# Performance work log

Measured on AMD Instinct MI355X. Metric: run time of the kernel, lower is better.

The kernel has to match this reference:

```python
import jax, jax.numpy as jnp
import numpy as np


def setup_inputs() -> dict:
    key = jax.random.key(0)
    ks = jax.random.split(key, 5)
    B, N, Fin, Fout = 8, 2048, 512, 512
    stdv = 1.0 / np.sqrt(Fout)
    w_stdv = 1.0 / np.sqrt(Fin)
    x = jax.random.normal(ks[0], (B, N, Fin), dtype=jnp.float32)
    weight = jax.random.uniform(ks[1], (Fin, Fout), dtype=jnp.float32, minval=-stdv, maxval=stdv)
    bias = jax.random.uniform(ks[2], (Fout,), dtype=jnp.float32, minval=-stdv, maxval=stdv)
    w_one = jax.random.uniform(ks[3], (Fin, Fin), dtype=jnp.float32, minval=-w_stdv, maxval=w_stdv)
    w_two = jax.random.uniform(ks[4], (Fin, Fin), dtype=jnp.float32, minval=-w_stdv, maxval=w_stdv)
    return {"x": x, "weight": weight, "bias": bias, "w_one": w_one, "w_two": w_two}


def reference(x, weight, bias, w_one, w_two):
    # x: [B, N, Fin]
    support = jnp.einsum('bnf,fo->bno', x, weight)          # [B, N, Fout]
    phi_one = jnp.einsum('ef,bnf->ben', w_one, x)           # [B, Fin, N]
    phi_two = jnp.einsum('ef,bnf->ben', w_two, x)           # [B, Fin, N]
    adj = jnp.einsum('ben,bem->bnm', phi_one, phi_two)      # [B, N, N]
    adj = jax.nn.softmax(adj, axis=1)                        # softmax over dim=1 (columns)
    out = jnp.einsum('bnm,bmo->bno', adj, support)           # [B, N, Fout]
    return out + bias
```

## Files before the change

kernel.cpp:

```cpp
#include <hip/hip_runtime.h>
#include <math.h>

#define BB 8
#define NN 2048
#define FF 512
#define LOG2E 1.4426950408889634f

typedef __attribute__((ext_vector_type(8))) short short8;
typedef __attribute__((ext_vector_type(4))) float floatx4;
typedef __attribute__((ext_vector_type(2))) float float2v;
typedef __attribute__((ext_vector_type(2))) __bf16 bf16x2;

__device__ __forceinline__ unsigned short f2bf(float f) {
    union { float f; unsigned u; } v; v.f = f;
    unsigned r = v.u + 0x7FFFu + ((v.u >> 16) & 1u);
    return (unsigned short)(r >> 16);
}

__device__ __forceinline__ float fexp2(float x) {
#if __has_builtin(__builtin_amdgcn_exp2f)
    return __builtin_amdgcn_exp2f(x);
#else
    return __expf(x * 0.69314718056f);
#endif
}

__device__ __forceinline__ void pk_store(unsigned short* p0, unsigned short* p1,
                                         float a, float b) {
    union { bf16x2 h; unsigned short s[2]; } u;
    float2v v; v.x = a; v.y = b;
    u.h = __builtin_convertvector(v, bf16x2);
    *p0 = u.s[0]; *p1 = u.s[1];
}

__global__ __launch_bounds__(256) void gemm_mfma_bt(
    const unsigned short* __restrict__ A, const unsigned short* __restrict__ B,
    void* __restrict__ Cv, const float* __restrict__ bias, float* __restrict__ Dsum,
    int M, int Nc, int K, int a_ld, int b_ld, int ldc,
    long a_batch, long b_batch, long c_batch, int mode)
{
    __shared__ __align__(16) unsigned short Alds[128 * 64];
    __shared__ __align__(16) unsigned short Blds[128 * 64];

    const int tid  = threadIdx.x;
    const int wave = tid >> 6;
    const int lane = tid & 63;
    const int bz   = blockIdx.z;

    const int m0 = blockIdx.y * 128;
    const int n0 = blockIdx.x * 128;

    const unsigned short* Aptr = A + (long)bz * a_batch + (long)m0 * a_ld;
    const unsigned short* Bptr = B + (long)bz * b_batch + (long)n0 * b_ld;

    const int wm   = (wave >> 1) * 64;
    const int wn   = (wave & 1) * 64;
    const int fl   = lane & 15;
    const int quad = lane >> 4;

    int offA[4], offB[4], cb[4];
    #pragma unroll
    for (int issue = 0; issue < 4; ++issue) {
        const int cbase = issue * 256 + wave * 64;
        const int c = cbase + lane;
        const int row = c >> 3;
        const int kq = ((c & 7) ^ ((c >> 3) & 7)) * 8;
        offA[issue] = row * a_ld + kq;
        offB[issue] = row * b_ld + kq;
        cb[issue] = cbase * 8;
    }

    floatx4 acc[4][4] = {};

    for (int k0 = 0; k0 < K; k0 += 64) {
        #pragma unroll
        for (int issue = 0; issue < 4; ++issue) {
            __builtin_amdgcn_global_load_lds(
                (const __attribute__((address_space(1))) void*)(Aptr + offA[issue]),
                (__attribute__((address_space(3))) void*)&Alds[cb[issue]], 16, 0, 0);
            __builtin_amdgcn_global_load_lds(
                (const __attribute__((address_space(1))) void*)(Bptr + offB[issue]),
                (__attribute__((address_space(3))) void*)&Blds[cb[issue]], 16, 0, 0);
        }
        Aptr += 64; Bptr += 64;
        __syncthreads();

        #pragma unroll
        for (int s = 0; s < 2; ++s) {
            short8 af[4], bf[4];
            const int slot = ((s * 4 + quad) ^ (fl & 7)) * 8;
            #pragma unroll
            for (int i = 0; i < 4; ++i)
                af[i] = *(const short8*)&Alds[(wm + i * 16 + fl) * 64 + slot];
            #pragma unroll
            for (int j = 0; j < 4; ++j)
                bf[j] = *(const short8*)&Blds[(wn + j * 16 + fl) * 64 + slot];
            #pragma unroll
            for (int i = 0; i < 4; ++i)
                #pragma unroll
                for (int j = 0; j < 4; ++j)
                    acc[i][j] = __builtin_amdgcn_mfma_f32_16x16x32_bf16(af[i], bf[j], acc[i][j], 0, 0, 0);
        }
        __syncthreads();
    }

    if (mode == 0) {
        float* Cb = (float*)Cv + (long)bz * c_batch;
        #pragma unroll
        for (int j = 0; j < 4; ++j) {
            const int ng = n0 + wn + j * 16 + fl;
            const float badd = bias ? bias[ng] : 0.0f;
            #pragma unroll
            for (int i = 0; i < 4; ++i) {
                const int mg = m0 + wm + i * 16 + quad * 4;
                #pragma unroll
                for (int r = 0; r < 4; ++r)
                    Cb[(long)(mg + r) * ldc + ng] = acc[i][j][r] + badd;
            }
        }
    } else if (mode == 1) {
        unsigned short* Cb = (unsigned short*)Cv + (long)bz * c_batch;
        #pragma unroll
        for (int j = 0; j < 4; ++j) {
            const int ng = n0 + wn + j * 16 + fl;
            #pragma unroll
            for (int i = 0; i < 4; ++i) {
                const int mg = m0 + wm + i * 16 + quad * 4;
                pk_store(&Cb[(long)(mg + 0) * ldc + ng], &Cb[(long)(mg + 1) * ldc + ng],
                         acc[i][j][0], acc[i][j][1]);
                pk_store(&Cb[(long)(mg + 2) * ldc + ng], &Cb[(long)(mg + 3) * ldc + ng],
                         acc[i][j][2], acc[i][j][3]);
            }
        }
    } else {
        unsigned short* Cb = (unsigned short*)Cv + (long)bz * c_batch;
        float* Db = Dsum + (long)bz * NN;
        #pragma unroll
        for (int i = 0; i < 4; ++i)
            #pragma unroll
            for (int j = 0; j < 4; ++j)
                #pragma unroll
                for (int r = 0; r < 4; ++r)
                    acc[i][j][r] = fexp2(acc[i][j][r]);
        #pragma unroll
        for (int j = 0; j < 4; ++j) {
            const int ng = n0 + wn + j * 16 + fl;
            float csum = 0.f;
            #pragma unroll
            for (int i = 0; i < 4; ++i) {
                const int mg = m0 + wm + i * 16 + quad * 4;
                csum += acc[i][j][0] + acc[i][j][1] + acc[i][j][2] + acc[i][j][3];
                pk_store(&Cb[(long)(mg + 0) * ldc + ng], &Cb[(long)(mg + 1) * ldc + ng],
                         acc[i][j][0], acc[i][j][1]);
                pk_store(&Cb[(long)(mg + 2) * ldc + ng], &Cb[(long)(mg + 3) * ldc + ng],
                         acc[i][j][2], acc[i][j][3]);
            }
            csum += __shfl_xor(csum, 16);
            csum += __shfl_xor(csum, 32);
            if (quad == 0) atomicAdd(&Db[ng], csum);
        }
    }
}

__global__ __launch_bounds__(256) void convert_all(
    const float* __restrict__ x, const float* __restrict__ w1, const float* __restrict__ w2,
    unsigned short* __restrict__ xb, unsigned short* __restrict__ w1b, unsigned short* __restrict__ w2b)
{
    const long NX = (long)BB * NN * FF / 8;
    const long NW = (long)FF * FF / 8;
    long t = (long)blockIdx.x * 256 + threadIdx.x;
    const float* in; unsigned short* out; float sc = 1.0f;
    if (t < NX) { in = x; out = xb; }
    else if (t < NX + NW) { in = w1; out = w1b; t -= NX; sc = LOG2E; }
    else if (t < NX + 2 * NW) { in = w2; out = w2b; t -= NX + NW; }
    else return;
    const long i = t * 8;
    float4 a = *(const float4*)(in + i);
    float4 b = *(const float4*)(in + i + 4);
    union { bf16x2 h[4]; short8 s8; } u;
    float2v v;
    v.x = a.x * sc; v.y = a.y * sc; u.h[0] = __builtin_convertvector(v, bf16x2);
    v.x = a.z * sc; v.y = a.w * sc; u.h[1] = __builtin_convertvector(v, bf16x2);
    v.x = b.x * sc; v.y = b.y * sc; u.h[2] = __builtin_convertvector(v, bf16x2);
    v.x = b.z * sc; v.y = b.w * sc; u.h[3] = __builtin_convertvector(v, bf16x2);
    *(short8*)(out + i) = u.s8;
}

__global__ __launch_bounds__(256) void transpose_convert(
    const float* __restrict__ in, unsigned short* __restrict__ out, int dim)
{
    __shared__ float t[32][33];
    const int tx = threadIdx.x & 31, ty = threadIdx.x >> 5;
    const int x0 = blockIdx.x * 32, y0 = blockIdx.y * 32;
    #pragma unroll
    for (int k = 0; k < 32; k += 8)
        t[ty + k][tx] = in[(long)(y0 + ty + k) * dim + x0 + tx];
    __syncthreads();
    #pragma unroll
    for (int k = 0; k < 32; k += 8)
        out[(long)(x0 + ty + k) * dim + y0 + tx] = f2bf(t[tx][ty + k]);
}

__global__ __launch_bounds__(256) void zero_f32(float* __restrict__ p, long n)
{
    long i = (long)blockIdx.x * 256 + threadIdx.x;
    if (i < n) p[i] = 0.0f;
}

__global__ __launch_bounds__(256) void scale_transpose(
    const unsigned short* __restrict__ Call, const float* __restrict__ D,
    unsigned short* __restrict__ supT, int batch0)
{
    __shared__ float t[32][33];
    __shared__ float rD[32];
    const int tx = threadIdx.x & 31, ty = threadIdx.x >> 5;
    const int mt = blockIdx.x * 32, ot = blockIdx.y * 32;
    const int b = batch0 + blockIdx.z;
    const unsigned short* Cb = Call + (long)b * NN * 1536;
    unsigned short* Tb = supT + (long)b * NN * FF;
    if (threadIdx.x < 32) rD[threadIdx.x] = 1.0f / D[(long)b * NN + mt + threadIdx.x];
    __syncthreads();
    #pragma unroll
    for (int k = 0; k < 32; k += 8) {
        unsigned short u = Cb[(long)(mt + ty + k) * 1536 + 1024 + ot + tx];
        union { unsigned uu; float f; } cv; cv.uu = ((unsigned)u) << 16;
        t[ty + k][tx] = cv.f;
    }
    __syncthreads();
    #pragma unroll
    for (int k = 0; k < 32; k += 8)
        Tb[(long)(ot + ty + k) * NN + mt + tx] = f2bf(t[tx][ty + k] * rD[tx]);
}

extern "C" void kernel_launch(void* const* d_in, const int* in_sizes, int n_in,
                              void* d_out, int out_size, void* d_ws, size_t ws_size,
                              hipStream_t stream)
{
    const float* x      = (const float*)d_in[0];
    const float* weight = (const float*)d_in[1];
    const float* bias   = (const float*)d_in[2];
    const float* w_one  = (const float*)d_in[3];
    const float* w_two  = (const float*)d_in[4];
    float* out = (float*)d_out;

    const long NF  = (long)NN * FF;
    const long NN2 = (long)NN * NN;
    const long CROW = 1536;

    char* p = (char*)d_ws;
    unsigned short* xb    = (unsigned short*)p; p += (size_t)BB * NF * 2;
    unsigned short* Wall  = (unsigned short*)p; p += (size_t)CROW * FF * 2;
    unsigned short* Call  = (unsigned short*)p; p += (size_t)BB * NN * CROW * 2;
    unsigned short* supT  = (unsigned short*)p; p += (size_t)BB * NF * 2;
    float*          Dsum  = (float*)p;          p += (size_t)BB * NN * 4;
    unsigned short* E     = (unsigned short*)p;
    unsigned short* w1b = Wall;
    unsigned short* w2b = Wall + (size_t)FF * FF;
    unsigned short* wTb = Wall + (size_t)2 * FF * FF;

    const size_t fixed = (size_t)(p - (char*)d_ws);
    const bool full = ws_size >= fixed + (size_t)BB * NN2 * 2;

    dim3 blk(256);

    convert_all<<<dim3(4352), blk, 0, stream>>>(x, w_one, w_two, xb, w1b, w2b);
    transpose_convert<<<dim3(FF / 32, FF / 32), blk, 0, stream>>>(weight, wTb, FF);
    zero_f32<<<dim3((BB * NN) / 256), blk, 0, stream>>>(Dsum, BB * NN);

    gemm_mfma_bt<<<dim3(CROW / 128, NN / 128, BB), blk, 0, stream>>>(
        xb, Wall, Call, nullptr, nullptr, NN, (int)CROW, FF,
        FF, FF, (int)CROW, NF, 0, NN * CROW, 1);

    if (full) {
        gemm_mfma_bt<<<dim3(NN / 128, NN / 128, BB), blk, 0, stream>>>(
            Call, Call + FF, E, nullptr, Dsum, NN, NN, FF,
            (int)CROW, (int)CROW, NN, NN * CROW, NN * CROW, NN2, 2);
        scale_transpose<<<dim3(NN / 32, FF / 32, BB), blk, 0, stream>>>(Call, Dsum, supT, 0);
        gemm_mfma_bt<<<dim3(FF / 128, NN / 128, BB), blk, 0, stream>>>(
            E, supT, out, bias, nullptr, NN, FF, NN,
            NN, NN, FF, NN2, NF, NF, 0);
    } else {
        for (int b = 0; b < BB; ++b) {
            const unsigned short* Cb = Call + (size_t)b * NN * CROW;
            gemm_mfma_bt<<<dim3(NN / 128, NN / 128, 1), blk, 0, stream>>>(
                Cb, Cb + FF, E, nullptr, Dsum + (size_t)b * NN, NN, NN, FF,
                (int)CROW, (int)CROW, NN, 0, 0, 0, 2);
            scale_transpose<<<dim3(NN / 32, FF / 32, 1), blk, 0, stream>>>(Call, Dsum, supT, b);
            gemm_mfma_bt<<<dim3(FF / 128, NN / 128, 1), blk, 0, stream>>>(
                E, supT + (size_t)b * NF, out + (size_t)b * NF, bias, nullptr, NN, FF, NN,
                NN, NN, FF, 0, 0, 0, 0);
        }
    }
}
```

Measured before the change: 240.6 us.

## Switch GEMMs to 32x32x16 MFMA with templated block tiles

Replaces the 16x16x32 bf16 MFMA kernel with a templated kernel that uses 32x32x16 MFMA instructions, each wave computing a 64x64 tile as 2x2 fragments. The template makes the block shape configurable: the first two GEMMs now use 8 waves with 256x128 tiles, and the final GEMM keeps 128x128 with 4 waves. Larger MFMA fragments mean fewer LDS fragment loads per FLOP, and the bigger tiles give more data reuse. The cost is more LDS per block and different occupancy. Epilogue indexing is rewritten to match the 32x32 accumulator layout.

```diff
diff --git a/kernel.cpp b/kernel.cpp
--- a/kernel.cpp
+++ b/kernel.cpp
@@ -7,7 +7,7 @@
 #define LOG2E 1.4426950408889634f
 
 typedef __attribute__((ext_vector_type(8))) short short8;
-typedef __attribute__((ext_vector_type(4))) float floatx4;
+typedef __attribute__((ext_vector_type(16))) float floatx16;
 typedef __attribute__((ext_vector_type(2))) float float2v;
 typedef __attribute__((ext_vector_type(2))) __bf16 bf16x2;
 
@@ -33,73 +33,85 @@
     *p0 = u.s[0]; *p1 = u.s[1];
 }
 
-__global__ __launch_bounds__(256) void gemm_mfma_bt(
+template<int WI, int WJ>
+__global__ __launch_bounds__(WI * WJ * 64) void gemm32(
     const unsigned short* __restrict__ A, const unsigned short* __restrict__ B,
     void* __restrict__ Cv, const float* __restrict__ bias, float* __restrict__ Dsum,
-    int M, int Nc, int K, int a_ld, int b_ld, int ldc,
+    int K, int a_ld, int b_ld, int ldc,
     long a_batch, long b_batch, long c_batch, int mode)
 {
-    __shared__ __align__(16) unsigned short Alds[128 * 64];
-    __shared__ __align__(16) unsigned short Blds[128 * 64];
+    constexpr int TI = WI * 64, TJ = WJ * 64, NT = WI * WJ * 64;
+    constexpr int AISS = TI * 8 / NT;
+    constexpr int BISS = TJ * 8 / NT;
+
+    __shared__ __align__(16) unsigned short Alds[TI * 64];
+    __shared__ __align__(16) unsigned short Blds[TJ * 64];
 
     const int tid  = threadIdx.x;
     const int wave = tid >> 6;
     const int lane = tid & 63;
     const int bz   = blockIdx.z;
 
-    const int m0 = blockIdx.y * 128;
-    const int n0 = blockIdx.x * 128;
+    const int m0 = blockIdx.y * TI;
+    const int n0 = blockIdx.x * TJ;
 
     const unsigned short* Aptr = A + (long)bz * a_batch + (long)m0 * a_ld;
     const unsigned short* Bptr = B + (long)bz * b_batch + (long)n0 * b_ld;
 
-    const int wm   = (wave >> 1) * 64;
-    const int wn   = (wave & 1) * 64;
-    const int fl   = lane & 15;
-    const int quad = lane >> 4;
-
-    int offA[4], offB[4], cb[4];
-    #pragma unroll
-    for (int issue = 0; issue < 4; ++issue) {
-        const int cbase = issue * 256 + wave * 64;
+    const int wi = wave / WJ, wj = wave % WJ;
+    const int wm = wi * 64, wn = wj * 64;
+    const int l31 = lane & 31;
+    const int lh  = lane >> 5;
+
+    int offA[AISS], cbA[AISS], offB[BISS], cbB[BISS];
+    #pragma unroll
+    for (int s = 0; s < AISS; ++s) {
+        const int cbase = s * NT + wave * 64;
         const int c = cbase + lane;
-        const int row = c >> 3;
-        const int kq = ((c & 7) ^ ((c >> 3) & 7)) * 8;
-        offA[issue] = row * a_ld + kq;
-        offB[issue] = row * b_ld + kq;
-        cb[issue] = cbase * 8;
-    }
-
-    floatx4 acc[4][4] = {};
+        offA[s] = (c >> 3) * a_ld + (((c & 7) ^ ((c >> 3) & 7)) << 3);
+        cbA[s] = cbase * 8;
+    }
+    #pragma unroll
+    for (int s = 0; s < BISS; ++s) {
+        const int cbase = s * NT + wave * 64;
+        const int c = cbase + lane;
+        offB[s] = (c >> 3) * b_ld + (((c & 7) ^ ((c >> 3) & 7)) << 3);
+        cbB[s] = cbase * 8;
+    }
+
+    floatx16 acc[2][2] = {};
 
     for (int k0 = 0; k0 < K; k0 += 64) {
         #pragma unroll
-        for (int issue = 0; issue < 4; ++issue) {
+        for (int s = 0; s < AISS; ++s)
             __builtin_amdgcn_global_load_lds(
-                (const __attribute__((address_space(1))) void*)(Aptr + offA[issue]),
-                (__attribute__((address_space(3))) void*)&Alds[cb[issue]], 16, 0, 0);
+                (const __attribute__((address_space(1))) void*)(Aptr + offA[s]),
+                (__attribute__((address_space(3))) void*)&Alds[cbA[s]], 16, 0, 0);
+        #pragma unroll
+        for (int s = 0; s < BISS; ++s)
             __builtin_amdgcn_global_load_lds(
-                (const __attribute__((address_space(1))) void*)(Bptr + offB[issue]),
-                (__attribute__((address_space(3))) void*)&Blds[cb[issue]], 16, 0, 0);
-        }
+                (const __attribute__((address_space(1))) void*)(Bptr + offB[s]),
+                (__attribute__((address_space(3))) void*)&Blds[cbB[s]], 16, 0, 0);
         Aptr += 64; Bptr += 64;
         __syncthreads();
 
         #pragma unroll
-        for (int s = 0; s < 2; ++s) {
-            short8 af[4], bf[4];
-            const int slot = ((s * 4 + quad) ^ (fl & 7)) * 8;
-            #pragma unroll
-            for (int i = 0; i < 4; ++i)
-                af[i] = *(const short8*)&Alds[(wm + i * 16 + fl) * 64 + slot];
-            #pragma unroll
-            for (int j = 0; j < 4; ++j)
-                bf[j] = *(const short8*)&Blds[(wn + j * 16 + fl) * 64 + slot];
-            #pragma unroll
-            for (int i = 0; i < 4; ++i)
-                #pragma unroll
-                for (int j = 0; j < 4; ++j)
-                    acc[i][j] = __builtin_amdgcn_mfma_f32_16x16x32_bf16(af[i], bf[j], acc[i][j], 0, 0, 0);
+        for (int ks = 0; ks < 4; ++ks) {
+            const int kc = ks * 2 + lh;
+            const int sw = (kc ^ (lane & 7)) << 3;
+            short8 af[2], bf[2];
+            #pragma unroll
+            for (int fi = 0; fi < 2; ++fi)
+                af[fi] = *(const short8*)&Alds[(wm + fi * 32 + l31) * 64 + sw];
+            #pragma unroll
+            for (int fj = 0; fj < 2; ++fj)
+                bf[fj] = *(const short8*)&Blds[(wn + fj * 32 + l31) * 64 + sw];
+            #pragma unroll
+            for (int fi = 0; fi < 2; ++fi)
+                #pragma unroll
+                for (int fj = 0; fj < 2; ++fj)
+                    acc[fi][fj] = __builtin_amdgcn_mfma_f32_32x32x16_bf16(
+                        af[fi], bf[fj], acc[fi][fj], 0, 0, 0);
         }
         __syncthreads();
     }
@@ -107,57 +119,64 @@
     if (mode == 0) {
         float* Cb = (float*)Cv + (long)bz * c_batch;
         #pragma unroll
-        for (int j = 0; j < 4; ++j) {
-            const int ng = n0 + wn + j * 16 + fl;
-            const float badd = bias ? bias[ng] : 0.0f;
-            #pragma unroll
-            for (int i = 0; i < 4; ++i) {
-                const int mg = m0 + wm + i * 16 + quad * 4;
-                #pragma unroll
-                for (int r = 0; r < 4; ++r)
-                    Cb[(long)(mg + r) * ldc + ng] = acc[i][j][r] + badd;
+        for (int fj = 0; fj < 2; ++fj) {
+            const int j = n0 + wn + fj * 32 + l31;
+            const float badd = bias ? bias[j] : 0.0f;
+            #pragma unroll
+            for (int fi = 0; fi < 2; ++fi) {
+                const int ib = m0 + wm + fi * 32 + 4 * lh;
+                #pragma unroll
+                for (int r = 0; r < 16; ++r) {
+                    const int i = ib + (r & 3) + 8 * (r >> 2);
+                    Cb[(long)i * ldc + j] = acc[fi][fj][r] + badd;
+                }
             }
         }
     } else if (mode == 1) {
         unsigned short* Cb = (unsigned short*)Cv + (long)bz * c_batch;
         #pragma unroll
-        for (int j = 0; j < 4; ++j) {
-            const int ng = n0 + wn + j * 16 + fl;
-            #pragma unroll
-            for (int i = 0; i < 4; ++i) {
-                const int mg = m0 + wm + i * 16 + quad * 4;
-                pk_store(&Cb[(long)(mg + 0) * ldc + ng], &Cb[(long)(mg + 1) * ldc + ng],
-                         acc[i][j][0], acc[i][j][1]);
-                pk_store(&Cb[(long)(mg + 2) * ldc + ng], &Cb[(long)(mg + 3) * ldc + ng],
-                         acc[i][j][2], acc[i][j][3]);
+        for (int fj = 0; fj < 2; ++fj) {
+            const int j = n0 + wn + fj * 32 + l31;
+            #pragma unroll
+            for (int fi = 0; fi < 2; ++fi) {
+                const int ib = m0 + wm + fi * 32 + 4 * lh;
+                #pragma unroll
+                for (int r = 0; r < 16; r += 2) {
+                    const int i0 = ib + ((r) & 3) + 8 * ((r) >> 2);
+                    const int i1 = ib + ((r + 1) & 3) + 8 * ((r + 1) >> 2);
+                    pk_store(&Cb[(long)i0 * ldc + j], &Cb[(long)i1 * ldc + j],
+                             acc[fi][fj][r], acc[fi][fj][r + 1]);
+                }
             }
         }
     } else {
         unsigned short* Cb = (unsigned short*)Cv + (long)bz * c_batch;
         float* Db = Dsum + (long)bz * NN;
         #pragma unroll
-        for (int i = 0; i < 4; ++i)
-            #pragma unroll
-            for (int j = 0; j < 4; ++j)
-                #pragma unroll
-                for (int r = 0; r < 4; ++r)
-                    acc[i][j][r] = fexp2(acc[i][j][r]);
-        #pragma unroll
-        for (int j = 0; j < 4; ++j) {
-            const int ng = n0 + wn + j * 16 + fl;
+        for (int fi = 0; fi < 2; ++fi)
+            #pragma unroll
+            for (int fj = 0; fj < 2; ++fj)
+                #pragma unroll
+                for (int r = 0; r < 16; ++r)
+                    acc[fi][fj][r] = fexp2(acc[fi][fj][r]);
+        #pragma unroll
+        for (int fj = 0; fj < 2; ++fj) {
+            const int j = n0 + wn + fj * 32 + l31;
             float csum = 0.f;
             #pragma unroll
-            for (int i = 0; i < 4; ++i) {
-                const int mg = m0 + wm + i * 16 + quad * 4;
-                csum += acc[i][j][0] + acc[i][j][1] + acc[i][j][2] + acc[i][j][3];
-                pk_store(&Cb[(long)(mg + 0) * ldc + ng], &Cb[(long)(mg + 1) * ldc + ng],
-                         acc[i][j][0], acc[i][j][1]);
-                pk_store(&Cb[(long)(mg + 2) * ldc + ng], &Cb[(long)(mg + 3) * ldc + ng],
-                         acc[i][j][2], acc[i][j][3]);
+            for (int fi = 0; fi < 2; ++fi) {
+                const int ib = m0 + wm + fi * 32 + 4 * lh;
+                #pragma unroll
+                for (int r = 0; r < 16; r += 2) {
+                    const int i0 = ib + ((r) & 3) + 8 * ((r) >> 2);
+                    const int i1 = ib + ((r + 1) & 3) + 8 * ((r + 1) >> 2);
+                    pk_store(&Cb[(long)i0 * ldc + j], &Cb[(long)i1 * ldc + j],
+                             acc[fi][fj][r], acc[fi][fj][r + 1]);
+                    csum += acc[fi][fj][r] + acc[fi][fj][r + 1];
+                }
             }
-            csum += __shfl_xor(csum, 16);
             csum += __shfl_xor(csum, 32);
-            if (quad == 0) atomicAdd(&Db[ng], csum);
+            if (lh == 0) atomicAdd(&Db[j], csum);
         }
     }
 }
@@ -267,27 +286,27 @@
     transpose_convert<<<dim3(FF / 32, FF / 32), blk, 0, stream>>>(weight, wTb, FF);
     zero_f32<<<dim3((BB * NN) / 256), blk, 0, stream>>>(Dsum, BB * NN);
 
-    gemm_mfma_bt<<<dim3(CROW / 128, NN / 128, BB), blk, 0, stream>>>(
-        xb, Wall, Call, nullptr, nullptr, NN, (int)CROW, FF,
+    gemm32<4, 2><<<dim3(CROW / 128, NN / 256, BB), dim3(512), 0, stream>>>(
+        xb, Wall, Call, nullptr, nullptr, FF,
         FF, FF, (int)CROW, NF, 0, NN * CROW, 1);
 
     if (full) {
-        gemm_mfma_bt<<<dim3(NN / 128, NN / 128, BB), blk, 0, stream>>>(
-            Call, Call + FF, E, nullptr, Dsum, NN, NN, FF,
+        gemm32<4, 2><<<dim3(NN / 128, NN / 256, BB), dim3(512), 0, stream>>>(
+            Call, Call + FF, E, nullptr, Dsum, FF,
             (int)CROW, (int)CROW, NN, NN * CROW, NN * CROW, NN2, 2);
         scale_transpose<<<dim3(NN / 32, FF / 32, BB), blk, 0, stream>>>(Call, Dsum, supT, 0);
-        gemm_mfma_bt<<<dim3(FF / 128, NN / 128, BB), blk, 0, stream>>>(
-            E, supT, out, bias, nullptr, NN, FF, NN,
+        gemm32<2, 2><<<dim3(FF / 128, NN / 128, BB), blk, 0, stream>>>(
+            E, supT, out, bias, nullptr, NN,
             NN, NN, FF, NN2, NF, NF, 0);
     } else {
         for (int b = 0; b < BB; ++b) {
             const unsigned short* Cb = Call + (size_t)b * NN * CROW;
-            gemm_mfma_bt<<<dim3(NN / 128, NN / 128, 1), blk, 0, stream>>>(
-                Cb, Cb + FF, E, nullptr, Dsum + (size_t)b * NN, NN, NN, FF,
+            gemm32<4, 2><<<dim3(NN / 128, NN / 256, 1), dim3(512), 0, stream>>>(
+                Cb, Cb + FF, E, nullptr, Dsum + (size_t)b * NN, FF,
                 (int)CROW, (int)CROW, NN, 0, 0, 0, 2);
             scale_transpose<<<dim3(NN / 32, FF / 32, 1), blk, 0, stream>>>(Call, Dsum, supT, b);
-            gemm_mfma_bt<<<dim3(FF / 128, NN / 128, 1), blk, 0, stream>>>(
-                E, supT + (size_t)b * NF, out + (size_t)b * NF, bias, nullptr, NN, FF, NN,
+            gemm32<2, 2><<<dim3(FF / 128, NN / 128, 1), blk, 0, stream>>>(
+                E, supT + (size_t)b * NF, out + (size_t)b * NF, bias, nullptr, NN,
                 NN, NN, FF, 0, 0, 0, 0);
         }
     }
```

Result: slower. 250.2 us (+4.0%).

## Use two-wave 128x128 GEMM blocks with 128x64 per-wave tiles

Applied to the files above, without the earlier changes.

The GEMM kernel now runs with 128 threads (2 waves) per 128x128 tile instead of 4 waves. Each wave computes a 128x64 sub-tile with an 8x4 grid of 16x16 MFMA accumulators. This raises the MFMA-to-LDS-read ratio, since A fragments are shared across more B fragments, and launch bounds request 2 blocks per CU. The trade-off is doubled accumulator register pressure and fewer waves per block for hiding latency, with each thread issuing twice as many global-to-LDS loads.

```diff
diff --git a/kernel.cpp b/kernel.cpp
--- a/kernel.cpp
+++ b/kernel.cpp
@@ -33,10 +33,10 @@
     *p0 = u.s[0]; *p1 = u.s[1];
 }
 
-__global__ __launch_bounds__(256) void gemm_mfma_bt(
+__global__ __launch_bounds__(128, 2) void gemm_bt16(
     const unsigned short* __restrict__ A, const unsigned short* __restrict__ B,
     void* __restrict__ Cv, const float* __restrict__ bias, float* __restrict__ Dsum,
-    int M, int Nc, int K, int a_ld, int b_ld, int ldc,
+    int K, int a_ld, int b_ld, int ldc,
     long a_batch, long b_batch, long c_batch, int mode)
 {
     __shared__ __align__(16) unsigned short Alds[128 * 64];
@@ -53,50 +53,47 @@
     const unsigned short* Aptr = A + (long)bz * a_batch + (long)m0 * a_ld;
     const unsigned short* Bptr = B + (long)bz * b_batch + (long)n0 * b_ld;
 
-    const int wm   = (wave >> 1) * 64;
-    const int wn   = (wave & 1) * 64;
+    const int wn   = wave * 64;
     const int fl   = lane & 15;
     const int quad = lane >> 4;
 
-    int offA[4], offB[4], cb[4];
-    #pragma unroll
-    for (int issue = 0; issue < 4; ++issue) {
-        const int cbase = issue * 256 + wave * 64;
-        const int c = cbase + lane;
+    int offA[8], offB[8];
+    #pragma unroll
+    for (int s = 0; s < 8; ++s) {
+        const int c = s * 128 + tid;
         const int row = c >> 3;
-        const int kq = ((c & 7) ^ ((c >> 3) & 7)) * 8;
-        offA[issue] = row * a_ld + kq;
-        offB[issue] = row * b_ld + kq;
-        cb[issue] = cbase * 8;
-    }
-
-    floatx4 acc[4][4] = {};
+        const int kq = ((c & 7) ^ (row & 7)) << 3;
+        offA[s] = row * a_ld + kq;
+        offB[s] = row * b_ld + kq;
+    }
+
+    floatx4 acc[8][4] = {};
 
     for (int k0 = 0; k0 < K; k0 += 64) {
         #pragma unroll
-        for (int issue = 0; issue < 4; ++issue) {
+        for (int s = 0; s < 8; ++s) {
             __builtin_amdgcn_global_load_lds(
-                (const __attribute__((address_space(1))) void*)(Aptr + offA[issue]),
-                (__attribute__((address_space(3))) void*)&Alds[cb[issue]], 16, 0, 0);
+                (const __attribute__((address_space(1))) void*)(Aptr + offA[s]),
+                (__attribute__((address_space(3))) void*)&Alds[(s * 128 + tid - lane) * 8], 16, 0, 0);
             __builtin_amdgcn_global_load_lds(
-                (const __attribute__((address_space(1))) void*)(Bptr + offB[issue]),
-                (__attribute__((address_space(3))) void*)&Blds[cb[issue]], 16, 0, 0);
+                (const __attribute__((address_space(1))) void*)(Bptr + offB[s]),
+                (__attribute__((address_space(3))) void*)&Blds[(s * 128 + tid - lane) * 8], 16, 0, 0);
         }
         Aptr += 64; Bptr += 64;
         __syncthreads();
 
         #pragma unroll
         for (int s = 0; s < 2; ++s) {
-            short8 af[4], bf[4];
             const int slot = ((s * 4 + quad) ^ (fl & 7)) * 8;
-            #pragma unroll
-            for (int i = 0; i < 4; ++i)
-                af[i] = *(const short8*)&Alds[(wm + i * 16 + fl) * 64 + slot];
+            short8 af[8], bf[4];
             #pragma unroll
             for (int j = 0; j < 4; ++j)
                 bf[j] = *(const short8*)&Blds[(wn + j * 16 + fl) * 64 + slot];
             #pragma unroll
-            for (int i = 0; i < 4; ++i)
+            for (int i = 0; i < 8; ++i)
+                af[i] = *(const short8*)&Alds[(i * 16 + fl) * 64 + slot];
+            #pragma unroll
+            for (int i = 0; i < 8; ++i)
                 #pragma unroll
                 for (int j = 0; j < 4; ++j)
                     acc[i][j] = __builtin_amdgcn_mfma_f32_16x16x32_bf16(af[i], bf[j], acc[i][j], 0, 0, 0);
@@ -111,8 +108,8 @@
             const int ng = n0 + wn + j * 16 + fl;
             const float badd = bias ? bias[ng] : 0.0f;
             #pragma unroll
-            for (int i = 0; i < 4; ++i) {
-                const int mg = m0 + wm + i * 16 + quad * 4;
+            for (int i = 0; i < 8; ++i) {
+                const int mg = m0 + i * 16 + quad * 4;
                 #pragma unroll
                 for (int r = 0; r < 4; ++r)
                     Cb[(long)(mg + r) * ldc + ng] = acc[i][j][r] + badd;
@@ -124,8 +121,8 @@
         for (int j = 0; j < 4; ++j) {
             const int ng = n0 + wn + j * 16 + fl;
             #pragma unroll
-            for (int i = 0; i < 4; ++i) {
-                const int mg = m0 + wm + i * 16 + quad * 4;
+            for (int i = 0; i < 8; ++i) {
+                const int mg = m0 + i * 16 + quad * 4;
                 pk_store(&Cb[(long)(mg + 0) * ldc + ng], &Cb[(long)(mg + 1) * ldc + ng],
                          acc[i][j][0], acc[i][j][1]);
                 pk_store(&Cb[(long)(mg + 2) * ldc + ng], &Cb[(long)(mg + 3) * ldc + ng],
@@ -136,7 +133,7 @@
         unsigned short* Cb = (unsigned short*)Cv + (long)bz * c_batch;
         float* Db = Dsum + (long)bz * NN;
         #pragma unroll
-        for (int i = 0; i < 4; ++i)
+        for (int i = 0; i < 8; ++i)
             #pragma unroll
             for (int j = 0; j < 4; ++j)
                 #pragma unroll
@@ -147,8 +144,8 @@
             const int ng = n0 + wn + j * 16 + fl;
             float csum = 0.f;
             #pragma unroll
-            for (int i = 0; i < 4; ++i) {
-                const int mg = m0 + wm + i * 16 + quad * 4;
+            for (int i = 0; i < 8; ++i) {
+                const int mg = m0 + i * 16 + quad * 4;
                 csum += acc[i][j][0] + acc[i][j][1] + acc[i][j][2] + acc[i][j][3];
                 pk_store(&Cb[(long)(mg + 0) * ldc + ng], &Cb[(long)(mg + 1) * ldc + ng],
                          acc[i][j][0], acc[i][j][1]);
@@ -262,32 +259,33 @@
     const bool full = ws_size >= fixed + (size_t)BB * NN2 * 2;
 
     dim3 blk(256);
+    dim3 gblk(128);
 
     convert_all<<<dim3(4352), blk, 0, stream>>>(x, w_one, w_two, xb, w1b, w2b);
     transpose_convert<<<dim3(FF / 32, FF / 32), blk, 0, stream>>>(weight, wTb, FF);
     zero_f32<<<dim3((BB * NN) / 256), blk, 0, stream>>>(Dsum, BB * NN);
 
-    gemm_mfma_bt<<<dim3(CROW / 128, NN / 128, BB), blk, 0, stream>>>(
-        xb, Wall, Call, nullptr, nullptr, NN, (int)CROW, FF,
+    gemm_bt16<<<dim3(CROW / 128, NN / 128, BB), gblk, 0, stream>>>(
+        xb, Wall, Call, nullptr, nullptr, FF,
         FF, FF, (int)CROW, NF, 0, NN * CROW, 1);
 
     if (full) {
-        gemm_mfma_bt<<<dim3(NN / 128, NN / 128, BB), blk, 0, stream>>>(
-            Call, Call + FF, E, nullptr, Dsum, NN, NN, FF,
+        gemm_bt16<<<dim3(NN / 128, NN / 128, BB), gblk, 0, stream>>>(
+            Call, Call + FF, E, nullptr, Dsum, FF,
             (int)CROW, (int)CROW, NN, NN * CROW, NN * CROW, NN2, 2);
         scale_transpose<<<dim3(NN / 32, FF / 32, BB), blk, 0, stream>>>(Call, Dsum, supT, 0);
-        gemm_mfma_bt<<<dim3(FF / 128, NN / 128, BB), blk, 0, stream>>>(
-            E, supT, out, bias, nullptr, NN, FF, NN,
+        gemm_bt16<<<dim3(FF / 128, NN / 128, BB), gblk, 0, stream>>>(
+            E, supT, out, bias, nullptr, NN,
             NN, NN, FF, NN2, NF, NF, 0);
     } else {
         for (int b = 0; b < BB; ++b) {
             const unsigned short* Cb = Call + (size_t)b * NN * CROW;
-            gemm_mfma_bt<<<dim3(NN / 128, NN / 128, 1), blk, 0, stream>>>(
-                Cb, Cb + FF, E, nullptr, Dsum + (size_t)b * NN, NN, NN, FF,
+            gemm_bt16<<<dim3(NN / 128, NN / 128, 1), gblk, 0, stream>>>(
+                Cb, Cb + FF, E, nullptr, Dsum + (size_t)b * NN, FF,
                 (int)CROW, (int)CROW, NN, 0, 0, 0, 2);
             scale_transpose<<<dim3(NN / 32, FF / 32, 1), blk, 0, stream>>>(Call, Dsum, supT, b);
-            gemm_mfma_bt<<<dim3(FF / 128, NN / 128, 1), blk, 0, stream>>>(
-                E, supT + (size_t)b * NF, out + (size_t)b * NF, bias, nullptr, NN, FF, NN,
+            gemm_bt16<<<dim3(FF / 128, NN / 128, 1), gblk, 0, stream>>>(
+                E, supT + (size_t)b * NF, out + (size_t)b * NF, bias, nullptr, NN,
                 NN, NN, FF, 0, 0, 0, 0);
         }
     }
```

New measurement: 242.6 us. No clear change (+0.8%).
